# Kernel tuning notes

Measured on AMD Instinct MI355X. Metric: run time of the kernel, lower is better.

Reference implementation:

```python
import jax, jax.numpy as jnp
import numpy as np

N, XDIM, D, K = 400000, 128, 3, 4
TWO_PI = 2.0 * np.pi


def _scaled(k, shape):
    fan_in = shape[0]
    return jax.random.normal(k, shape, jnp.float32) * np.float32(1.0 / np.sqrt(fan_in))


def setup_inputs() -> dict:
    key = jax.random.key(0)
    ks = jax.random.split(key, 9)
    return {
        "x1": jax.random.normal(ks[0], (N, XDIM), jnp.float32),
        "enc_w1": _scaled(ks[1], (XDIM, 16)), "enc_b1": jnp.zeros((16,), jnp.float32),
        "enc_w2": _scaled(ks[2], (16, 8)),   "enc_b2": jnp.zeros((8,), jnp.float32),
        "enc_w3": _scaled(ks[3], (8, 1)),    "enc_b3": jnp.zeros((1,), jnp.float32),
        "dec_w1": _scaled(ks[4], (1, 8)),    "dec_b1": jnp.zeros((8,), jnp.float32),
        "dec_w2": _scaled(ks[5], (8, 16)),   "dec_b2": jnp.zeros((16,), jnp.float32),
        "dec_w3": _scaled(ks[6], (16, XDIM)),"dec_b3": jnp.zeros((XDIM,), jnp.float32),
        "est_w1": _scaled(ks[7], (D, 8)),    "est_b1": jnp.zeros((8,), jnp.float32),
        "est_w2": _scaled(ks[8], (8, K)),    "est_b2": jnp.zeros((K,), jnp.float32),
    }


def reference(x1, enc_w1, enc_b1, enc_w2, enc_b2, enc_w3, enc_b3,
              dec_w1, dec_b1, dec_w2, dec_b2, dec_w3, dec_b3,
              est_w1, est_b1, est_w2, est_b2):
    # encoder: Dense(16,tanh)->Dense(8,tanh)->Dense(1,tanh)
    h = jnp.tanh(x1 @ enc_w1 + enc_b1)
    h = jnp.tanh(h @ enc_w2 + enc_b2)
    z1 = jnp.tanh(h @ enc_w3 + enc_b3)            # [N,1]
    # decoder: Dense(8,tanh)->Dense(16,tanh)->Dense(xdim, linear)
    h = jnp.tanh(z1 @ dec_w1 + dec_b1)
    h = jnp.tanh(h @ dec_w2 + dec_b2)
    x2 = h @ dec_w3 + dec_b3                      # [N,xdim]

    # relative distances
    dist_cos = jnp.sum(x1 * x2, axis=1, keepdims=True) / (
        jnp.linalg.norm(x1, axis=1, keepdims=True) * jnp.linalg.norm(x2, axis=1, keepdims=True))
    dist_euc = jnp.linalg.norm(x1 - x2, axis=1, keepdims=True)
    z = jnp.concatenate([z1, dist_cos, dist_euc], axis=1)   # [N,D]

    # estimator: Dense(8,tanh)->Dense(K,softmax)
    gamma = jax.nn.softmax(jnp.tanh(z @ est_w1 + est_b1) @ est_w2 + est_b2)  # [N,K]

    # GMM parameters from soft assignments
    gamma_sum = jnp.sum(gamma, axis=0)                        # [K]
    phi = jnp.mean(gamma, axis=0)                             # [K]
    mu = jnp.einsum('ik,il->kl', gamma, z) / gamma_sum[:, None]          # [K,D]
    z_centered = jnp.sqrt(gamma)[:, :, None] * (z[:, None, :] - mu[None, :, :])  # [N,K,D]
    sigma = jnp.einsum('ikl,ikm->klm', z_centered, z_centered) / gamma_sum[:, None, None]  # [K,D,D]

    # per-sample energy
    z_mu = z[:, None, :] - mu[None, :, :]                     # [N,K,D]
    sigma_inv = jnp.linalg.inv(sigma)                         # [K,D,D]
    item1 = jnp.log(phi)[None, :]                             # [1,K]
    item2 = -0.5 * jnp.einsum('nkd,kde,nke->nk', z_mu, sigma_inv, z_mu)  # [N,K]
    sigma_det = jnp.linalg.det(TWO_PI * sigma)                # [K]
    item3 = jnp.log(jnp.sqrt(sigma_det))[None, :]             # [1,K]
    energy = -jnp.sum(item1 + item2 - item3, axis=1)          # [N]

    # loss
    lambda1, lambda2 = 0.01, 0.0001
    diag = jnp.diagonal(sigma, axis1=-2, axis2=-1)            # [K,D]
    loss3 = lambda2 * jnp.sum(1.0 / diag)
    loss2 = lambda1 * jnp.mean(energy)
    loss1 = jnp.mean(jnp.sum(jnp.square(x1 - x2), axis=1))
    loss = loss1 + loss2 + loss3
    return energy, loss
```

## Files before the change

### kernel.cpp

```cpp
#include <hip/hip_runtime.h>

#define NSAMP 400000
#define NBLK  1563


__device__ __forceinline__ float ftanh(float x) {
    float e = __expf(2.0f * x);
    return 1.0f - __fdividef(2.0f, e + 1.0f);
}

__global__ __launch_bounds__(256) void prep_kernel(const float* __restrict__ dw3,
                                                   const float* __restrict__ db3,
                                                   float* __restrict__ Gm,
                                                   float* __restrict__ gv,
                                                   float* __restrict__ bb) {
    int t = threadIdx.x;
    int a = t >> 4, b = t & 15;
    float s = 0.f;
    for (int j = 0; j < 128; ++j) s += dw3[a * 128 + j] * dw3[b * 128 + j];
    Gm[t] = s;
    if (t < 16) {
        float sg = 0.f;
        for (int j = 0; j < 128; ++j) sg += dw3[t * 128 + j] * db3[j];
        gv[t] = sg;
    }
    if (t == 0) {
        float sbv = 0.f;
        for (int j = 0; j < 128; ++j) sbv += db3[j] * db3[j];
        *bb = sbv;
    }
}

__global__ __launch_bounds__(256) void pass1_kernel(
    const float* __restrict__ x1,
    const float* __restrict__ ew1, const float* __restrict__ eb1,
    const float* __restrict__ ew2, const float* __restrict__ eb2,
    const float* __restrict__ ew3, const float* __restrict__ eb3,
    const float* __restrict__ dw1, const float* __restrict__ db1,
    const float* __restrict__ dw2, const float* __restrict__ db2,
    const float* __restrict__ dw3, const float* __restrict__ db3,
    const float* __restrict__ tw1, const float* __restrict__ tb1,
    const float* __restrict__ tw2, const float* __restrict__ tb2,
    const float* __restrict__ Gm, const float* __restrict__ gv,
    const float* __restrict__ bbp,
    double* __restrict__ acc, float4* __restrict__ zbuf) {
    int i = blockIdx.x * 256 + threadIdx.x;
    bool active = (i < NSAMP);
    int row = active ? i : 0;
    const float4* xr = (const float4*)(x1 + (size_t)row * 128);

    float u[16], v[16];
#pragma unroll
    for (int k = 0; k < 16; ++k) { u[k] = 0.f; v[k] = 0.f; }
    float s2 = 0.f, sb = 0.f;

    float4 buf[4];
#pragma unroll
    for (int c = 0; c < 4; ++c) buf[c] = xr[c];

#pragma unroll 1
    for (int blk = 0; blk < 8; ++blk) {
        float xe[16];
#pragma unroll
        for (int c = 0; c < 4; ++c) {
            xe[c * 4 + 0] = buf[c].x; xe[c * 4 + 1] = buf[c].y;
            xe[c * 4 + 2] = buf[c].z; xe[c * 4 + 3] = buf[c].w;
        }
        if (blk < 7) {
#pragma unroll
            for (int c = 0; c < 4; ++c) buf[c] = xr[(blk + 1) * 4 + c];
        }
        int j0 = blk * 16;
#pragma unroll
        for (int e = 0; e < 16; ++e) {
            float x = xe[e];
            s2 = fmaf(x, x, s2);
            sb = fmaf(x, db3[j0 + e], sb);
#pragma unroll
            for (int k = 0; k < 16; ++k) u[k] = fmaf(x, ew1[(j0 + e) * 16 + k], u[k]);
        }
#pragma unroll
        for (int q = 0; q < 16; ++q) {
            float a2 = v[q];
#pragma unroll
            for (int e = 0; e < 16; ++e) a2 = fmaf(xe[e], dw3[q * 128 + j0 + e], a2);
            v[q] = a2;
        }
    }

    float h1[16];
#pragma unroll
    for (int k = 0; k < 16; ++k) h1[k] = ftanh(u[k] + eb1[k]);
    float h2[8];
#pragma unroll
    for (int m = 0; m < 8; ++m) {
        float a2 = eb2[m];
#pragma unroll
        for (int k = 0; k < 16; ++k) a2 = fmaf(h1[k], ew2[k * 8 + m], a2);
        h2[m] = ftanh(a2);
    }
    float a3 = eb3[0];
#pragma unroll
    for (int m = 0; m < 8; ++m) a3 = fmaf(h2[m], ew3[m], a3);
    float z1 = ftanh(a3);

    float d1[8];
#pragma unroll
    for (int p = 0; p < 8; ++p) d1[p] = ftanh(fmaf(z1, dw1[p], db1[p]));
    float d2[16];
#pragma unroll
    for (int q = 0; q < 16; ++q) {
        float a2 = db2[q];
#pragma unroll
        for (int p = 0; p < 8; ++p) a2 = fmaf(d1[p], dw2[p * 16 + q], a2);
        d2[q] = ftanh(a2);
    }

    float dot = sb;
#pragma unroll
    for (int q = 0; q < 16; ++q) dot = fmaf(d2[q], v[q], dot);
    float n2 = *bbp;
#pragma unroll
    for (int a = 0; a < 16; ++a) {
        float ra = 2.0f * gv[a];
#pragma unroll
        for (int b = 0; b < 16; ++b) ra = fmaf(Gm[a * 16 + b], d2[b], ra);
        n2 = fmaf(d2[a], ra, n2);
    }
    n2 = fmaxf(n2, 1e-20f);
    float euc2 = fmaxf(s2 - 2.0f * dot + n2, 0.f);
    float deuc = sqrtf(euc2);
    float dcos = dot * rsqrtf(s2 * n2);

    float zf[3] = {z1, dcos, deuc};

    float e1[8];
#pragma unroll
    for (int p = 0; p < 8; ++p) {
        float a2 = tb1[p];
        a2 = fmaf(zf[0], tw1[0 * 8 + p], a2);
        a2 = fmaf(zf[1], tw1[1 * 8 + p], a2);
        a2 = fmaf(zf[2], tw1[2 * 8 + p], a2);
        e1[p] = ftanh(a2);
    }
    float lg[4];
#pragma unroll
    for (int k = 0; k < 4; ++k) {
        float a2 = tb2[k];
#pragma unroll
        for (int p = 0; p < 8; ++p) a2 = fmaf(e1[p], tw2[p * 4 + k], a2);
        lg[k] = a2;
    }
    float mx = fmaxf(fmaxf(lg[0], lg[1]), fmaxf(lg[2], lg[3]));
    float ex[4]; float se = 0.f;
#pragma unroll
    for (int k = 0; k < 4; ++k) { ex[k] = __expf(lg[k] - mx); se += ex[k]; }
    float inv = __fdividef(1.0f, se);
    float gam[4];
#pragma unroll
    for (int k = 0; k < 4; ++k) gam[k] = ex[k] * inv;

    if (active) zbuf[i] = make_float4(zf[0], zf[1], zf[2], 0.f);
    if (!active) { gam[0] = gam[1] = gam[2] = gam[3] = 0.f; euc2 = 0.f; }

    __shared__ float sPart[4][41];
    int lane = threadIdx.x & 63;
    int wid = threadIdx.x >> 6;

#define REDUCE_STORE(T, VAL) { float _v = (VAL);                          \
        _v += __shfl_down(_v, 32); _v += __shfl_down(_v, 16);             \
        _v += __shfl_down(_v, 8);  _v += __shfl_down(_v, 4);              \
        _v += __shfl_down(_v, 2);  _v += __shfl_down(_v, 1);              \
        if (lane == 0) sPart[wid][T] = _v; }

#pragma unroll
    for (int k = 0; k < 4; ++k) REDUCE_STORE(k, gam[k]);
#pragma unroll
    for (int k = 0; k < 4; ++k) {
#pragma unroll
        for (int d = 0; d < 3; ++d) REDUCE_STORE(4 + k * 3 + d, gam[k] * zf[d]);
    }
#pragma unroll
    for (int k = 0; k < 4; ++k) {
        REDUCE_STORE(16 + k * 6 + 0, gam[k] * zf[0] * zf[0]);
        REDUCE_STORE(16 + k * 6 + 1, gam[k] * zf[0] * zf[1]);
        REDUCE_STORE(16 + k * 6 + 2, gam[k] * zf[0] * zf[2]);
        REDUCE_STORE(16 + k * 6 + 3, gam[k] * zf[1] * zf[1]);
        REDUCE_STORE(16 + k * 6 + 4, gam[k] * zf[1] * zf[2]);
        REDUCE_STORE(16 + k * 6 + 5, gam[k] * zf[2] * zf[2]);
    }
    REDUCE_STORE(40, euc2);
#undef REDUCE_STORE

    __syncthreads();
    if (threadIdx.x < 41) {
        double s = (double)sPart[0][threadIdx.x] + (double)sPart[1][threadIdx.x]
                 + (double)sPart[2][threadIdx.x] + (double)sPart[3][threadIdx.x];
        unsafeAtomicAdd(&acc[threadIdx.x], s);
    }
}

__global__ void gmm_kernel(double* __restrict__ acc, float* __restrict__ P) {
    if (threadIdx.x != 0 || blockIdx.x != 0) return;
    double M[6] = {0, 0, 0, 0, 0, 0}, bv[3] = {0, 0, 0}, A = 0.0, loss3 = 0.0;
    const double TWO_PI = 6.283185307179586;
    for (int k = 0; k < 4; ++k) {
        double g = acc[k];
        double phi = g / (double)NSAMP;
        double mu0 = acc[4 + k * 3 + 0] / g;
        double mu1 = acc[4 + k * 3 + 1] / g;
        double mu2 = acc[4 + k * 3 + 2] / g;
        double S00 = acc[16 + k * 6 + 0] / g - mu0 * mu0;
        double S01 = acc[16 + k * 6 + 1] / g - mu0 * mu1;
        double S02 = acc[16 + k * 6 + 2] / g - mu0 * mu2;
        double S11 = acc[16 + k * 6 + 3] / g - mu1 * mu1;
        double S12 = acc[16 + k * 6 + 4] / g - mu1 * mu2;
        double S22 = acc[16 + k * 6 + 5] / g - mu2 * mu2;
        double c00 = S11 * S22 - S12 * S12;
        double c01 = S02 * S12 - S01 * S22;
        double c02 = S01 * S12 - S02 * S11;
        double det = S00 * c00 + S01 * c01 + S02 * c02;
        double id = 1.0 / det;
        double I00 = c00 * id, I01 = c01 * id, I02 = c02 * id;
        double I11 = (S00 * S22 - S02 * S02) * id;
        double I12 = (S01 * S02 - S00 * S12) * id;
        double I22 = (S00 * S11 - S01 * S01) * id;
        M[0] += I00; M[1] += I01; M[2] += I02; M[3] += I11; M[4] += I12; M[5] += I22;
        double b0 = I00 * mu0 + I01 * mu1 + I02 * mu2;
        double b1 = I01 * mu0 + I11 * mu1 + I12 * mu2;
        double b2 = I02 * mu0 + I12 * mu1 + I22 * mu2;
        bv[0] += b0; bv[1] += b1; bv[2] += b2;
        double quad = mu0 * b0 + mu1 * b1 + mu2 * b2;
        A += -log(phi) + 0.5 * log(TWO_PI * TWO_PI * TWO_PI * det) + 0.5 * quad;
        loss3 += 1e-4 * (1.0 / S00 + 1.0 / S11 + 1.0 / S22);
    }
    P[0] = (float)M[0]; P[1] = (float)M[1]; P[2] = (float)M[2];
    P[3] = (float)M[3]; P[4] = (float)M[4]; P[5] = (float)M[5];
    P[6] = (float)bv[0]; P[7] = (float)bv[1]; P[8] = (float)bv[2];
    P[9] = (float)A;
    acc[42] = acc[40] / (double)NSAMP + loss3;
}

__global__ __launch_bounds__(256) void energy_kernel(const float4* __restrict__ zbuf,
                                                     const float* __restrict__ P,
                                                     double* __restrict__ acc,
                                                     float* __restrict__ out) {
    int i = blockIdx.x * 256 + threadIdx.x;
    float e = 0.f;
    if (i < NSAMP) {
        float4 z4 = zbuf[i];
        float z0 = z4.x, z1 = z4.y, z2 = z4.z;
        float q = P[0] * z0 * z0 + P[3] * z1 * z1 + P[5] * z2 * z2
                + 2.f * (P[1] * z0 * z1 + P[2] * z0 * z2 + P[4] * z1 * z2);
        e = P[9] + 0.5f * q - (P[6] * z0 + P[7] * z1 + P[8] * z2);
        out[i] = e;
    }
    float s = e;
    s += __shfl_down(s, 32); s += __shfl_down(s, 16); s += __shfl_down(s, 8);
    s += __shfl_down(s, 4);  s += __shfl_down(s, 2);  s += __shfl_down(s, 1);
    __shared__ float sE[4];
    if ((threadIdx.x & 63) == 0) sE[threadIdx.x >> 6] = s;
    __syncthreads();
    if (threadIdx.x == 0) {
        double t = (double)sE[0] + (double)sE[1] + (double)sE[2] + (double)sE[3];
        unsafeAtomicAdd(&acc[41], t);
    }
}

__global__ void final_kernel(const double* __restrict__ acc, float* __restrict__ out) {
    if (threadIdx.x == 0 && blockIdx.x == 0)
        out[NSAMP] = (float)(acc[42] + 0.01 * acc[41] / (double)NSAMP);
}

extern "C" void kernel_launch(void* const* d_in, const int* in_sizes, int n_in,
                              void* d_out, int out_size, void* d_ws, size_t ws_size,
                              hipStream_t stream) {
    const float* x1  = (const float*)d_in[0];
    const float* ew1 = (const float*)d_in[1];
    const float* eb1 = (const float*)d_in[2];
    const float* ew2 = (const float*)d_in[3];
    const float* eb2 = (const float*)d_in[4];
    const float* ew3 = (const float*)d_in[5];
    const float* eb3 = (const float*)d_in[6];
    const float* dw1 = (const float*)d_in[7];
    const float* db1 = (const float*)d_in[8];
    const float* dw2 = (const float*)d_in[9];
    const float* db2 = (const float*)d_in[10];
    const float* dw3 = (const float*)d_in[11];
    const float* db3 = (const float*)d_in[12];
    const float* tw1 = (const float*)d_in[13];
    const float* tb1 = (const float*)d_in[14];
    const float* tw2 = (const float*)d_in[15];
    const float* tb2 = (const float*)d_in[16];
    float* out = (float*)d_out;
    char* ws = (char*)d_ws;
    double* acc = (double*)ws;
    float* P    = (float*)(ws + 384);
    float* Gm   = (float*)(ws + 1024);
    float* gv   = (float*)(ws + 2048);
    float* bb   = (float*)(ws + 2112);
    float4* zb  = (float4*)(ws + 4096);

    hipMemsetAsync(d_ws, 0, 512, stream);
    prep_kernel<<<1, 256, 0, stream>>>(dw3, db3, Gm, gv, bb);
    pass1_kernel<<<NBLK, 256, 0, stream>>>(x1, ew1, eb1, ew2, eb2, ew3, eb3,
                                           dw1, db1, dw2, db2, dw3, db3,
                                           tw1, tb1, tw2, tb2, Gm, gv, bb, acc, zb);
    gmm_kernel<<<1, 64, 0, stream>>>(acc, P);
    energy_kernel<<<NBLK, 256, 0, stream>>>(zb, P, acc, out);
    final_kernel<<<1, 64, 0, stream>>>(acc, out);
}
```

Before: 456.8 us.

## Stage x1 chunks through double-buffered shared memory for coalesced loads

```diff
diff --git a/kernel.cpp b/kernel.cpp
--- a/kernel.cpp
+++ b/kernel.cpp
@@ -31,6 +31,8 @@
     }
 }
 
+#define TSTRIDE 20
+
 __global__ __launch_bounds__(256) void pass1_kernel(
     const float* __restrict__ x1,
     const float* __restrict__ ew1, const float* __restrict__ eb1,
@@ -44,32 +46,58 @@
     const float* __restrict__ Gm, const float* __restrict__ gv,
     const float* __restrict__ bbp,
     double* __restrict__ acc, float4* __restrict__ zbuf) {
-    int i = blockIdx.x * 256 + threadIdx.x;
+    __shared__ float tile[2][256 * TSTRIDE];
+
+    int t = threadIdx.x;
+    int i = blockIdx.x * 256 + t;
     bool active = (i < NSAMP);
-    int row = active ? i : 0;
-    const float4* xr = (const float4*)(x1 + (size_t)row * 128);
+
+    int srow = t >> 2;
+    int sc4 = t & 3;
+
+    {
+#pragma unroll
+        for (int s = 0; s < 4; ++s) {
+            int row = srow + 64 * s;
+            int grow = blockIdx.x * 256 + row;
+            if (grow >= NSAMP) grow = NSAMP - 1;
+            float4 val = *(const float4*)(x1 + (size_t)grow * 128 + sc4 * 4);
+            *(float4*)(&tile[0][row * TSTRIDE + sc4 * 4]) = val;
+        }
+    }
+    __syncthreads();
 
     float u[16], v[16];
 #pragma unroll
     for (int k = 0; k < 16; ++k) { u[k] = 0.f; v[k] = 0.f; }
     float s2 = 0.f, sb = 0.f;
 
-    float4 buf[4];
-#pragma unroll
-    for (int c = 0; c < 4; ++c) buf[c] = xr[c];
-
 #pragma unroll 1
     for (int blk = 0; blk < 8; ++blk) {
+        int cur = blk & 1;
+
+        float4 st[4];
+        if (blk < 7) {
+#pragma unroll
+            for (int s = 0; s < 4; ++s) {
+                int row = srow + 64 * s;
+                int grow = blockIdx.x * 256 + row;
+                if (grow >= NSAMP) grow = NSAMP - 1;
+                st[s] = *(const float4*)(x1 + (size_t)grow * 128 + (blk + 1) * 16 + sc4 * 4);
+            }
+        }
+
         float xe[16];
-#pragma unroll
-        for (int c = 0; c < 4; ++c) {
-            xe[c * 4 + 0] = buf[c].x; xe[c * 4 + 1] = buf[c].y;
-            xe[c * 4 + 2] = buf[c].z; xe[c * 4 + 3] = buf[c].w;
-        }
-        if (blk < 7) {
-#pragma unroll
-            for (int c = 0; c < 4; ++c) buf[c] = xr[(blk + 1) * 4 + c];
-        }
+        {
+            const float* base = &tile[cur][t * TSTRIDE];
+#pragma unroll
+            for (int c = 0; c < 4; ++c) {
+                float4 a4 = *(const float4*)(base + c * 4);
+                xe[c * 4 + 0] = a4.x; xe[c * 4 + 1] = a4.y;
+                xe[c * 4 + 2] = a4.z; xe[c * 4 + 3] = a4.w;
+            }
+        }
+
         int j0 = blk * 16;
 #pragma unroll
         for (int e = 0; e < 16; ++e) {
@@ -86,6 +114,15 @@
             for (int e = 0; e < 16; ++e) a2 = fmaf(xe[e], dw3[q * 128 + j0 + e], a2);
             v[q] = a2;
         }
+
+        if (blk < 7) {
+#pragma unroll
+            for (int s = 0; s < 4; ++s) {
+                int row = srow + 64 * s;
+                *(float4*)(&tile[cur ^ 1][row * TSTRIDE + sc4 * 4]) = st[s];
+            }
+        }
+        __syncthreads();
     }
 
     float h1[16];
```

After: 598.2 us. +31.0%, slower.

## Stage x1 rows through LDS with async global_load_lds and fold prep/final kernels

Applied to the files above, without the earlier changes.

```diff
diff --git a/kernel.cpp b/kernel.cpp
--- a/kernel.cpp
+++ b/kernel.cpp
@@ -9,25 +9,25 @@
     return 1.0f - __fdividef(2.0f, e + 1.0f);
 }
 
-__global__ __launch_bounds__(256) void prep_kernel(const float* __restrict__ dw3,
-                                                   const float* __restrict__ db3,
-                                                   float* __restrict__ Gm,
-                                                   float* __restrict__ gv,
-                                                   float* __restrict__ bb) {
-    int t = threadIdx.x;
-    int a = t >> 4, b = t & 15;
-    float s = 0.f;
-    for (int j = 0; j < 128; ++j) s += dw3[a * 128 + j] * dw3[b * 128 + j];
-    Gm[t] = s;
-    if (t < 16) {
-        float sg = 0.f;
-        for (int j = 0; j < 128; ++j) sg += dw3[t * 128 + j] * db3[j];
-        gv[t] = sg;
-    }
-    if (t == 0) {
-        float sbv = 0.f;
-        for (int j = 0; j < 128; ++j) sbv += db3[j] * db3[j];
-        *bb = sbv;
+__device__ __forceinline__ void gl_lds16(const float* g, float* l) {
+    __builtin_amdgcn_global_load_lds(
+        (const __attribute__((address_space(1))) void*)(g),
+        (__attribute__((address_space(3))) void*)(l), 16, 0, 0);
+}
+
+__device__ __forceinline__ void stage_chunk(const float* __restrict__ x1,
+                                            float* buf, int block_base,
+                                            int t, int chunk) {
+#pragma unroll
+    for (int s = 0; s < 4; ++s) {
+        int q = s * 256 + t;
+        int r = q >> 2;
+        int c = (q & 3) ^ ((q >> 3) & 3);
+        int grow = block_base + r;
+        if (grow >= NSAMP) grow = NSAMP - 1;
+        const float* src = x1 + (size_t)grow * 128 + chunk * 16 + c * 4;
+        float* dst = buf + (size_t)(s * 256 + (t & ~63)) * 4;
+        gl_lds16(src, dst);
     }
 }
 
@@ -41,35 +41,60 @@
     const float* __restrict__ dw3, const float* __restrict__ db3,
     const float* __restrict__ tw1, const float* __restrict__ tb1,
     const float* __restrict__ tw2, const float* __restrict__ tb2,
-    const float* __restrict__ Gm, const float* __restrict__ gv,
-    const float* __restrict__ bbp,
     double* __restrict__ acc, float4* __restrict__ zbuf) {
-    int i = blockIdx.x * 256 + threadIdx.x;
+    __shared__ float tileA[1024 * 4];
+    __shared__ float tileB[1024 * 4];
+    __shared__ float sGm[256];
+    __shared__ float sgv[16];
+    __shared__ float sbb;
+    __shared__ float sPart[4][41];
+
+    int t = threadIdx.x;
+    int i = blockIdx.x * 256 + t;
+    int block_base = blockIdx.x * 256;
     bool active = (i < NSAMP);
-    int row = active ? i : 0;
-    const float4* xr = (const float4*)(x1 + (size_t)row * 128);
+
+    stage_chunk(x1, tileA, block_base, t, 0);
+
+    {
+        int a = t >> 4, b = t & 15;
+        float s = 0.f;
+        for (int j = 0; j < 128; ++j) s = fmaf(dw3[a * 128 + j], dw3[b * 128 + j], s);
+        sGm[t] = s;
+        if (t >= 64 && t < 80) {
+            float sg = 0.f;
+            for (int j = 0; j < 128; ++j) sg = fmaf(dw3[(t - 64) * 128 + j], db3[j], sg);
+            sgv[t - 64] = sg;
+        }
+        if (t == 128) {
+            float sv = 0.f;
+            for (int j = 0; j < 128; ++j) sv = fmaf(db3[j], db3[j], sv);
+            sbb = sv;
+        }
+    }
+    __syncthreads();
 
     float u[16], v[16];
 #pragma unroll
     for (int k = 0; k < 16; ++k) { u[k] = 0.f; v[k] = 0.f; }
     float s2 = 0.f, sb = 0.f;
 
-    float4 buf[4];
-#pragma unroll
-    for (int c = 0; c < 4; ++c) buf[c] = xr[c];
+    int sw = (t >> 1) & 3;
+    float* cur = tileA;
+    float* nxt = tileB;
 
 #pragma unroll 1
     for (int blk = 0; blk < 8; ++blk) {
+        if (blk < 7) stage_chunk(x1, nxt, block_base, t, blk + 1);
+
         float xe[16];
 #pragma unroll
         for (int c = 0; c < 4; ++c) {
-            xe[c * 4 + 0] = buf[c].x; xe[c * 4 + 1] = buf[c].y;
-            xe[c * 4 + 2] = buf[c].z; xe[c * 4 + 3] = buf[c].w;
-        }
-        if (blk < 7) {
-#pragma unroll
-            for (int c = 0; c < 4; ++c) buf[c] = xr[(blk + 1) * 4 + c];
-        }
+            float4 a4 = *(const float4*)(cur + t * 16 + ((c ^ sw) * 4));
+            xe[c * 4 + 0] = a4.x; xe[c * 4 + 1] = a4.y;
+            xe[c * 4 + 2] = a4.z; xe[c * 4 + 3] = a4.w;
+        }
+
         int j0 = blk * 16;
 #pragma unroll
         for (int e = 0; e < 16; ++e) {
@@ -86,6 +111,9 @@
             for (int e = 0; e < 16; ++e) a2 = fmaf(xe[e], dw3[q * 128 + j0 + e], a2);
             v[q] = a2;
         }
+
+        float* tmp = cur; cur = nxt; nxt = tmp;
+        __syncthreads();
     }
 
     float h1[16];
@@ -119,12 +147,12 @@
     float dot = sb;
 #pragma unroll
     for (int q = 0; q < 16; ++q) dot = fmaf(d2[q], v[q], dot);
-    float n2 = *bbp;
+    float n2 = sbb;
 #pragma unroll
     for (int a = 0; a < 16; ++a) {
-        float ra = 2.0f * gv[a];
-#pragma unroll
-        for (int b = 0; b < 16; ++b) ra = fmaf(Gm[a * 16 + b], d2[b], ra);
+        float ra = 2.0f * sgv[a];
+#pragma unroll
+        for (int b = 0; b < 16; ++b) ra = fmaf(sGm[a * 16 + b], d2[b], ra);
         n2 = fmaf(d2[a], ra, n2);
     }
     n2 = fmaxf(n2, 1e-20f);
@@ -163,7 +191,6 @@
     if (active) zbuf[i] = make_float4(zf[0], zf[1], zf[2], 0.f);
     if (!active) { gam[0] = gam[1] = gam[2] = gam[3] = 0.f; euc2 = 0.f; }
 
-    __shared__ float sPart[4][41];
     int lane = threadIdx.x & 63;
     int wid = threadIdx.x >> 6;
 
@@ -264,12 +291,13 @@
     if (threadIdx.x == 0) {
         double t = (double)sE[0] + (double)sE[1] + (double)sE[2] + (double)sE[3];
         unsafeAtomicAdd(&acc[41], t);
-    }
-}
-
-__global__ void final_kernel(const double* __restrict__ acc, float* __restrict__ out) {
-    if (threadIdx.x == 0 && blockIdx.x == 0)
-        out[NSAMP] = (float)(acc[42] + 0.01 * acc[41] / (double)NSAMP);
+        __threadfence();
+        unsigned tk = atomicAdd((unsigned int*)(acc + 44), 1u);
+        if (tk == NBLK - 1) {
+            double esum = unsafeAtomicAdd(&acc[41], 0.0);
+            out[NSAMP] = (float)(acc[42] + 0.01 * esum / (double)NSAMP);
+        }
+    }
 }
 
 extern "C" void kernel_launch(void* const* d_in, const int* in_sizes, int n_in,
@@ -295,18 +323,13 @@
     float* out = (float*)d_out;
     char* ws = (char*)d_ws;
     double* acc = (double*)ws;
-    float* P    = (float*)(ws + 384);
-    float* Gm   = (float*)(ws + 1024);
-    float* gv   = (float*)(ws + 2048);
-    float* bb   = (float*)(ws + 2112);
+    float* P    = (float*)(ws + 512);
     float4* zb  = (float4*)(ws + 4096);
 
     hipMemsetAsync(d_ws, 0, 512, stream);
-    prep_kernel<<<1, 256, 0, stream>>>(dw3, db3, Gm, gv, bb);
     pass1_kernel<<<NBLK, 256, 0, stream>>>(x1, ew1, eb1, ew2, eb2, ew3, eb3,
                                            dw1, db1, dw2, db2, dw3, db3,
-                                           tw1, tb1, tw2, tb2, Gm, gv, bb, acc, zb);
+                                           tw1, tb1, tw2, tb2, acc, zb);
     gmm_kernel<<<1, 64, 0, stream>>>(acc, P);
     energy_kernel<<<NBLK, 256, 0, stream>>>(zb, P, acc, out);
-    final_kernel<<<1, 64, 0, stream>>>(acc, out);
-}
+}
```

After: 477.4 us. +4.5%, slower.

## Split rows across four waves with LDS staging and per-block partial reductions

Applied to the files above, without the earlier changes.

```diff
diff --git a/kernel.cpp b/kernel.cpp
--- a/kernel.cpp
+++ b/kernel.cpp
@@ -1,12 +1,20 @@
 #include <hip/hip_runtime.h>
 
 #define NSAMP 400000
-#define NBLK  1563
+#define ROWS_PER_BLK 64
+#define NBLK1 6250
+#define NBLK_E 1563
 
 
 __device__ __forceinline__ float ftanh(float x) {
     float e = __expf(2.0f * x);
     return 1.0f - __fdividef(2.0f, e + 1.0f);
+}
+
+__device__ __forceinline__ void gl_lds16(const float* g, float* l) {
+    __builtin_amdgcn_global_load_lds(
+        (const __attribute__((address_space(1))) void*)(g),
+        (__attribute__((address_space(3))) void*)(l), 16, 0, 0);
 }
 
 __global__ __launch_bounds__(256) void prep_kernel(const float* __restrict__ dw3,
@@ -17,21 +25,21 @@
     int t = threadIdx.x;
     int a = t >> 4, b = t & 15;
     float s = 0.f;
-    for (int j = 0; j < 128; ++j) s += dw3[a * 128 + j] * dw3[b * 128 + j];
+    for (int j = 0; j < 128; ++j) s = fmaf(dw3[a * 128 + j], dw3[b * 128 + j], s);
     Gm[t] = s;
     if (t < 16) {
         float sg = 0.f;
-        for (int j = 0; j < 128; ++j) sg += dw3[t * 128 + j] * db3[j];
+        for (int j = 0; j < 128; ++j) sg = fmaf(dw3[t * 128 + j], db3[j], sg);
         gv[t] = sg;
     }
     if (t == 0) {
-        float sbv = 0.f;
-        for (int j = 0; j < 128; ++j) sbv += db3[j] * db3[j];
-        *bb = sbv;
-    }
-}
-
-__global__ __launch_bounds__(256) void pass1_kernel(
+        float sv = 0.f;
+        for (int j = 0; j < 128; ++j) sv = fmaf(db3[j], db3[j], sv);
+        *bb = sv;
+    }
+}
+
+__global__ __launch_bounds__(256, 4) void pass1_kernel(
     const float* __restrict__ x1,
     const float* __restrict__ ew1, const float* __restrict__ eb1,
     const float* __restrict__ ew2, const float* __restrict__ eb2,
@@ -43,54 +51,97 @@
     const float* __restrict__ tw2, const float* __restrict__ tb2,
     const float* __restrict__ Gm, const float* __restrict__ gv,
     const float* __restrict__ bbp,
-    double* __restrict__ acc, float4* __restrict__ zbuf) {
-    int i = blockIdx.x * 256 + threadIdx.x;
-    bool active = (i < NSAMP);
-    int row = active ? i : 0;
-    const float4* xr = (const float4*)(x1 + (size_t)row * 128);
+    float* __restrict__ Pp, float4* __restrict__ zbuf) {
+    __shared__ float lds[9216];
+
+    int t = threadIdx.x;
+    int w = t >> 6;
+    int lane = t & 63;
+    int blk = blockIdx.x;
+    size_t rowbase = (size_t)blk * ROWS_PER_BLK;
+
+#pragma unroll
+    for (int k = 0; k < 8; ++k) {
+        int i = w * 8 + k;
+        int r = 2 * i + (lane >> 5);
+        const float* src = x1 + (rowbase + r) * 128 + (lane & 31) * 4;
+        gl_lds16(src, &lds[i * 260]);
+    }
+    __syncthreads();
+
+    float xr[32];
+    {
+        int sbase = (lane >> 1) * 65 + (lane & 1) * 32 + w * 8;
+#pragma unroll
+        for (int m = 0; m < 8; ++m) {
+            float4 a4 = *(const float4*)&lds[(sbase + m) * 4];
+            xr[m * 4 + 0] = a4.x; xr[m * 4 + 1] = a4.y;
+            xr[m * 4 + 2] = a4.z; xr[m * 4 + 3] = a4.w;
+        }
+    }
 
     float u[16], v[16];
 #pragma unroll
     for (int k = 0; k < 16; ++k) { u[k] = 0.f; v[k] = 0.f; }
     float s2 = 0.f, sb = 0.f;
-
-    float4 buf[4];
-#pragma unroll
-    for (int c = 0; c < 4; ++c) buf[c] = xr[c];
-
-#pragma unroll 1
-    for (int blk = 0; blk < 8; ++blk) {
-        float xe[16];
-#pragma unroll
-        for (int c = 0; c < 4; ++c) {
-            xe[c * 4 + 0] = buf[c].x; xe[c * 4 + 1] = buf[c].y;
-            xe[c * 4 + 2] = buf[c].z; xe[c * 4 + 3] = buf[c].w;
+    int c0 = w * 32;
+#pragma unroll
+    for (int e = 0; e < 32; ++e) {
+        float x = xr[e];
+        int c = c0 + e;
+        s2 = fmaf(x, x, s2);
+        sb = fmaf(x, db3[c], sb);
+#pragma unroll
+        for (int k = 0; k < 16; ++k) u[k] = fmaf(x, ew1[c * 16 + k], u[k]);
+    }
+#pragma unroll
+    for (int q = 0; q < 16; ++q) {
+        float a2 = v[q];
+#pragma unroll
+        for (int e = 0; e < 32; ++e) a2 = fmaf(xr[e], dw3[q * 128 + c0 + e], a2);
+        v[q] = a2;
+    }
+
+    __syncthreads();
+    {
+        int pb = (w * 64 + lane) * 9;
+        *(float4*)&lds[(pb + 0) * 4] = make_float4(u[0], u[1], u[2], u[3]);
+        *(float4*)&lds[(pb + 1) * 4] = make_float4(u[4], u[5], u[6], u[7]);
+        *(float4*)&lds[(pb + 2) * 4] = make_float4(u[8], u[9], u[10], u[11]);
+        *(float4*)&lds[(pb + 3) * 4] = make_float4(u[12], u[13], u[14], u[15]);
+        *(float4*)&lds[(pb + 4) * 4] = make_float4(v[0], v[1], v[2], v[3]);
+        *(float4*)&lds[(pb + 5) * 4] = make_float4(v[4], v[5], v[6], v[7]);
+        *(float4*)&lds[(pb + 6) * 4] = make_float4(v[8], v[9], v[10], v[11]);
+        *(float4*)&lds[(pb + 7) * 4] = make_float4(v[12], v[13], v[14], v[15]);
+        *(float4*)&lds[(pb + 8) * 4] = make_float4(s2, sb, 0.f, 0.f);
+    }
+    __syncthreads();
+
+    if (t >= 64) return;
+
+    float U[16], V[16];
+#pragma unroll
+    for (int k = 0; k < 16; ++k) { U[k] = 0.f; V[k] = 0.f; }
+    float S2 = 0.f, SB = 0.f;
+#pragma unroll
+    for (int p = 0; p < 4; ++p) {
+        int base = (p * 64 + t) * 9;
+#pragma unroll
+        for (int c4 = 0; c4 < 4; ++c4) {
+            float4 a4 = *(const float4*)&lds[(base + c4) * 4];
+            U[c4 * 4 + 0] += a4.x; U[c4 * 4 + 1] += a4.y;
+            U[c4 * 4 + 2] += a4.z; U[c4 * 4 + 3] += a4.w;
+            float4 b4 = *(const float4*)&lds[(base + 4 + c4) * 4];
+            V[c4 * 4 + 0] += b4.x; V[c4 * 4 + 1] += b4.y;
+            V[c4 * 4 + 2] += b4.z; V[c4 * 4 + 3] += b4.w;
         }
-        if (blk < 7) {
-#pragma unroll
-            for (int c = 0; c < 4; ++c) buf[c] = xr[(blk + 1) * 4 + c];
-        }
-        int j0 = blk * 16;
-#pragma unroll
-        for (int e = 0; e < 16; ++e) {
-            float x = xe[e];
-            s2 = fmaf(x, x, s2);
-            sb = fmaf(x, db3[j0 + e], sb);
-#pragma unroll
-            for (int k = 0; k < 16; ++k) u[k] = fmaf(x, ew1[(j0 + e) * 16 + k], u[k]);
-        }
-#pragma unroll
-        for (int q = 0; q < 16; ++q) {
-            float a2 = v[q];
-#pragma unroll
-            for (int e = 0; e < 16; ++e) a2 = fmaf(xe[e], dw3[q * 128 + j0 + e], a2);
-            v[q] = a2;
-        }
+        float4 s4 = *(const float4*)&lds[(base + 8) * 4];
+        S2 += s4.x; SB += s4.y;
     }
 
     float h1[16];
 #pragma unroll
-    for (int k = 0; k < 16; ++k) h1[k] = ftanh(u[k] + eb1[k]);
+    for (int k = 0; k < 16; ++k) h1[k] = ftanh(U[k] + eb1[k]);
     float h2[8];
 #pragma unroll
     for (int m = 0; m < 8; ++m) {
@@ -116,9 +167,9 @@
         d2[q] = ftanh(a2);
     }
 
-    float dot = sb;
-#pragma unroll
-    for (int q = 0; q < 16; ++q) dot = fmaf(d2[q], v[q], dot);
+    float dot = SB;
+#pragma unroll
+    for (int q = 0; q < 16; ++q) dot = fmaf(d2[q], V[q], dot);
     float n2 = *bbp;
 #pragma unroll
     for (int a = 0; a < 16; ++a) {
@@ -128,9 +179,9 @@
         n2 = fmaf(d2[a], ra, n2);
     }
     n2 = fmaxf(n2, 1e-20f);
-    float euc2 = fmaxf(s2 - 2.0f * dot + n2, 0.f);
+    float euc2 = fmaxf(S2 - 2.0f * dot + n2, 0.f);
     float deuc = sqrtf(euc2);
-    float dcos = dot * rsqrtf(s2 * n2);
+    float dcos = dot * rsqrtf(S2 * n2);
 
     float zf[3] = {z1, dcos, deuc};
 
@@ -160,62 +211,68 @@
 #pragma unroll
     for (int k = 0; k < 4; ++k) gam[k] = ex[k] * inv;
 
-    if (active) zbuf[i] = make_float4(zf[0], zf[1], zf[2], 0.f);
-    if (!active) { gam[0] = gam[1] = gam[2] = gam[3] = 0.f; euc2 = 0.f; }
-
-    __shared__ float sPart[4][41];
-    int lane = threadIdx.x & 63;
-    int wid = threadIdx.x >> 6;
-
-#define REDUCE_STORE(T, VAL) { float _v = (VAL);                          \
+    zbuf[rowbase + t] = make_float4(zf[0], zf[1], zf[2], 0.f);
+
+#define RED(T, VAL) { float _v = (VAL);                                   \
         _v += __shfl_down(_v, 32); _v += __shfl_down(_v, 16);             \
         _v += __shfl_down(_v, 8);  _v += __shfl_down(_v, 4);              \
-        _v += __shfl_down(_v, 2);  _v += __shfl_down(_v, 1);              \
-        if (lane == 0) sPart[wid][T] = _v; }
-
-#pragma unroll
-    for (int k = 0; k < 4; ++k) REDUCE_STORE(k, gam[k]);
+        _v += __shfl_down(_v, 2);  _v += __shfl_down(_v, 1);             \
+        if (t == 0) Pp[(T) * NBLK1 + blk] = _v; }
+
+#pragma unroll
+    for (int k = 0; k < 4; ++k) RED(k, gam[k]);
 #pragma unroll
     for (int k = 0; k < 4; ++k) {
 #pragma unroll
-        for (int d = 0; d < 3; ++d) REDUCE_STORE(4 + k * 3 + d, gam[k] * zf[d]);
+        for (int d = 0; d < 3; ++d) RED(4 + k * 3 + d, gam[k] * zf[d]);
     }
 #pragma unroll
     for (int k = 0; k < 4; ++k) {
-        REDUCE_STORE(16 + k * 6 + 0, gam[k] * zf[0] * zf[0]);
-        REDUCE_STORE(16 + k * 6 + 1, gam[k] * zf[0] * zf[1]);
-        REDUCE_STORE(16 + k * 6 + 2, gam[k] * zf[0] * zf[2]);
-        REDUCE_STORE(16 + k * 6 + 3, gam[k] * zf[1] * zf[1]);
-        REDUCE_STORE(16 + k * 6 + 4, gam[k] * zf[1] * zf[2]);
-        REDUCE_STORE(16 + k * 6 + 5, gam[k] * zf[2] * zf[2]);
-    }
-    REDUCE_STORE(40, euc2);
-#undef REDUCE_STORE
-
-    __syncthreads();
-    if (threadIdx.x < 41) {
-        double s = (double)sPart[0][threadIdx.x] + (double)sPart[1][threadIdx.x]
-                 + (double)sPart[2][threadIdx.x] + (double)sPart[3][threadIdx.x];
-        unsafeAtomicAdd(&acc[threadIdx.x], s);
-    }
-}
-
-__global__ void gmm_kernel(double* __restrict__ acc, float* __restrict__ P) {
-    if (threadIdx.x != 0 || blockIdx.x != 0) return;
+        RED(16 + k * 6 + 0, gam[k] * zf[0] * zf[0]);
+        RED(16 + k * 6 + 1, gam[k] * zf[0] * zf[1]);
+        RED(16 + k * 6 + 2, gam[k] * zf[0] * zf[2]);
+        RED(16 + k * 6 + 3, gam[k] * zf[1] * zf[1]);
+        RED(16 + k * 6 + 4, gam[k] * zf[1] * zf[2]);
+        RED(16 + k * 6 + 5, gam[k] * zf[2] * zf[2]);
+    }
+    RED(40, euc2);
+#undef RED
+}
+
+__global__ __launch_bounds__(256) void gmm_kernel(const float* __restrict__ Pp,
+                                                  double* __restrict__ acc,
+                                                  float* __restrict__ P) {
+    int v = blockIdx.x;
+    double s = 0.0;
+    for (int i = threadIdx.x; i < NBLK1; i += 256) s += (double)Pp[v * NBLK1 + i];
+    s += __shfl_down(s, 32); s += __shfl_down(s, 16); s += __shfl_down(s, 8);
+    s += __shfl_down(s, 4);  s += __shfl_down(s, 2);  s += __shfl_down(s, 1);
+    __shared__ double sd[4];
+    if ((threadIdx.x & 63) == 0) sd[threadIdx.x >> 6] = s;
+    __syncthreads();
+    if (threadIdx.x != 0) return;
+    double tot = sd[0] + sd[1] + sd[2] + sd[3];
+    unsafeAtomicAdd(&acc[v], tot);
+    __threadfence();
+    unsigned tk = atomicAdd((unsigned int*)(acc + 46), 1u);
+    if (tk != 40) return;
+
+    double a[41];
+    for (int j = 0; j < 41; ++j) a[j] = unsafeAtomicAdd(&acc[j], 0.0);
     double M[6] = {0, 0, 0, 0, 0, 0}, bv[3] = {0, 0, 0}, A = 0.0, loss3 = 0.0;
     const double TWO_PI = 6.283185307179586;
     for (int k = 0; k < 4; ++k) {
-        double g = acc[k];
+        double g = a[k];
         double phi = g / (double)NSAMP;
-        double mu0 = acc[4 + k * 3 + 0] / g;
-        double mu1 = acc[4 + k * 3 + 1] / g;
-        double mu2 = acc[4 + k * 3 + 2] / g;
-        double S00 = acc[16 + k * 6 + 0] / g - mu0 * mu0;
-        double S01 = acc[16 + k * 6 + 1] / g - mu0 * mu1;
-        double S02 = acc[16 + k * 6 + 2] / g - mu0 * mu2;
-        double S11 = acc[16 + k * 6 + 3] / g - mu1 * mu1;
-        double S12 = acc[16 + k * 6 + 4] / g - mu1 * mu2;
-        double S22 = acc[16 + k * 6 + 5] / g - mu2 * mu2;
+        double mu0 = a[4 + k * 3 + 0] / g;
+        double mu1 = a[4 + k * 3 + 1] / g;
+        double mu2 = a[4 + k * 3 + 2] / g;
+        double S00 = a[16 + k * 6 + 0] / g - mu0 * mu0;
+        double S01 = a[16 + k * 6 + 1] / g - mu0 * mu1;
+        double S02 = a[16 + k * 6 + 2] / g - mu0 * mu2;
+        double S11 = a[16 + k * 6 + 3] / g - mu1 * mu1;
+        double S12 = a[16 + k * 6 + 4] / g - mu1 * mu2;
+        double S22 = a[16 + k * 6 + 5] / g - mu2 * mu2;
         double c00 = S11 * S22 - S12 * S12;
         double c01 = S02 * S12 - S01 * S22;
         double c02 = S01 * S12 - S02 * S11;
@@ -238,7 +295,7 @@
     P[3] = (float)M[3]; P[4] = (float)M[4]; P[5] = (float)M[5];
     P[6] = (float)bv[0]; P[7] = (float)bv[1]; P[8] = (float)bv[2];
     P[9] = (float)A;
-    acc[42] = acc[40] / (double)NSAMP + loss3;
+    unsafeAtomicAdd(&acc[42], a[40] / (double)NSAMP + loss3);
 }
 
 __global__ __launch_bounds__(256) void energy_kernel(const float4* __restrict__ zbuf,
@@ -264,12 +321,14 @@
     if (threadIdx.x == 0) {
         double t = (double)sE[0] + (double)sE[1] + (double)sE[2] + (double)sE[3];
         unsafeAtomicAdd(&acc[41], t);
-    }
-}
-
-__global__ void final_kernel(const double* __restrict__ acc, float* __restrict__ out) {
-    if (threadIdx.x == 0 && blockIdx.x == 0)
-        out[NSAMP] = (float)(acc[42] + 0.01 * acc[41] / (double)NSAMP);
+        __threadfence();
+        unsigned tk = atomicAdd((unsigned int*)(acc + 44), 1u);
+        if (tk == NBLK_E - 1) {
+            double esum = unsafeAtomicAdd(&acc[41], 0.0);
+            double lpart = unsafeAtomicAdd(&acc[42], 0.0);
+            out[NSAMP] = (float)(lpart + 0.01 * esum / (double)NSAMP);
+        }
+    }
 }
 
 extern "C" void kernel_launch(void* const* d_in, const int* in_sizes, int n_in,
@@ -295,18 +354,18 @@
     float* out = (float*)d_out;
     char* ws = (char*)d_ws;
     double* acc = (double*)ws;
-    float* P    = (float*)(ws + 384);
+    float* P    = (float*)(ws + 512);
     float* Gm   = (float*)(ws + 1024);
     float* gv   = (float*)(ws + 2048);
     float* bb   = (float*)(ws + 2112);
-    float4* zb  = (float4*)(ws + 4096);
+    float* Pp   = (float*)(ws + 4096);
+    float4* zb  = (float4*)(ws + 2097152);
 
     hipMemsetAsync(d_ws, 0, 512, stream);
     prep_kernel<<<1, 256, 0, stream>>>(dw3, db3, Gm, gv, bb);
-    pass1_kernel<<<NBLK, 256, 0, stream>>>(x1, ew1, eb1, ew2, eb2, ew3, eb3,
-                                           dw1, db1, dw2, db2, dw3, db3,
-                                           tw1, tb1, tw2, tb2, Gm, gv, bb, acc, zb);
-    gmm_kernel<<<1, 64, 0, stream>>>(acc, P);
-    energy_kernel<<<NBLK, 256, 0, stream>>>(zb, P, acc, out);
-    final_kernel<<<1, 64, 0, stream>>>(acc, out);
-}
+    pass1_kernel<<<NBLK1, 256, 0, stream>>>(x1, ew1, eb1, ew2, eb2, ew3, eb3,
+                                            dw1, db1, dw2, db2, dw3, db3,
+                                            tw1, tb1, tw2, tb2, Gm, gv, bb, Pp, zb);
+    gmm_kernel<<<41, 256, 0, stream>>>(Pp, acc, P);
+    energy_kernel<<<NBLK_E, 256, 0, stream>>>(zb, P, acc, out);
+}
```

After: 575.3 us. 1.26x slower.
